# Performance work log

Measured on AMD Instinct MI355X. Metric: run time of the kernel, lower is better.

The kernel has to match this reference:

```python
import jax, jax.numpy as jnp
import numpy as np

H = 384  # LSTMCell features per layer
REVS = (True, False, True, False, True)  # reverse flags per layer (keep_order=True restores order)


def _lstm_layer(x, Wi, Wh, b, rev):
    # x: [B, T, D]; Wi: [D, 4H]; Wh: [H, 4H]; b: [4H]
    # flax nn.RNN(reverse=True, keep_order=True) == flip input, scan, flip output.
    if rev:
        x = x[:, ::-1]
    xT = jnp.swapaxes(x, 0, 1)            # [T, B, D]
    xproj = xT @ Wi + b                    # precompute input projection: [T, B, 4H]
    B = x.shape[0]
    c0 = jnp.zeros((B, H), x.dtype)
    h0 = jnp.zeros((B, H), x.dtype)

    def step(carry, xp):
        c, h = carry
        z = xp + h @ Wh                    # [B, 4H]
        i, f, g, o = jnp.split(z, 4, axis=-1)
        c = jax.nn.sigmoid(f) * c + jax.nn.sigmoid(i) * jnp.tanh(g)
        h = jax.nn.sigmoid(o) * jnp.tanh(c)
        return (c, h), h

    _, hs = jax.lax.scan(step, (c0, h0), xproj)  # hs: [T, B, H]
    out = jnp.swapaxes(hs, 0, 1)                 # [B, T, H]
    if rev:
        out = out[:, ::-1]
    return out


def setup_inputs() -> dict:
    key = jax.random.key(0)
    k_x, k_wi, k_wh = jax.random.split(key, 3)
    B, T, D = 64, 1024, 384
    x = jax.random.normal(k_x, (B, T, D), dtype=jnp.float32)
    # flax LSTMCell: input dense (no bias) + recurrent dense (with bias); bias init zeros.
    Wi = jax.random.normal(k_wi, (5, D, 4 * H), dtype=jnp.float32) * 0.05
    Wh = jax.random.normal(k_wh, (5, H, 4 * H), dtype=jnp.float32) * 0.05
    b = jnp.zeros((5, 4 * H), dtype=jnp.float32)
    return {"x": x, "Wi": Wi, "Wh": Wh, "b": b}


def reference(x, Wi, Wh, b):
    for l, rev in enumerate(REVS):
        x = _lstm_layer(x, Wi[l], Wh[l], b[l], rev)
    return x
```

## Files before the change

### kernel.cpp

```cpp
#include <hip/hip_runtime.h>
#include <cstdint>
#include <cstddef>


#define T_SEQ   1024
#define DD      384
#define HH      384
#define FH      1536
#define NBATCH  64
#define BG      8
#define CC      24
#define JHW     16
#define RTHREADS 512
#define SMEM_BYTES 129664

typedef unsigned long long u64;

__device__ __forceinline__ float sigmoidf_(float x) {
  return 1.0f / (1.0f + __expf(-x));
}
__device__ __forceinline__ float tanhf_(float x) {
  float ax = fabsf(x);
  float e  = __expf(-2.0f * ax);
  float r  = (1.0f - e) / (1.0f + e);
  return (x >= 0.0f) ? r : -r;
}

__global__ __launch_bounds__(256) void gemm_xproj(
    const float* __restrict__ xin, const float* __restrict__ Wi,
    const float* __restrict__ bias, float* __restrict__ xproj,
    int t0, int rev)
{
  __shared__ float As[8][132];
  __shared__ float Bs[8][132];

  const int tid = threadIdx.x;
  const int tx = tid & 15, ty = tid >> 4;
  const int m0 = blockIdx.y * 128;
  const int j0 = blockIdx.x * 128;

  const int r    = tid >> 1;
  const int part = tid & 1;
  const int m    = m0 + r;
  const int b    = m & 63;
  const int trel = m >> 6;
  const int t    = t0 + trel;
  const int tsrc = rev ? (T_SEQ - 1 - t) : t;
  const float* arow = xin + ((size_t)b * T_SEQ + tsrc) * DD + part * 4;

  const int kr = tid >> 5;
  const int jc = (tid & 31) << 2;
  const float* brow = Wi + (size_t)kr * FH + j0 + jc;

  float acc[8][8];
#pragma unroll
  for (int i = 0; i < 8; ++i)
#pragma unroll
    for (int j = 0; j < 8; ++j) acc[i][j] = 0.0f;

  for (int kt = 0; kt < 48; ++kt) {
    float4 av = *(const float4*)(arow + kt * 8);
    float4 bv = *(const float4*)(brow + (size_t)kt * 8 * FH);
    __syncthreads();
    As[part * 4 + 0][r] = av.x;
    As[part * 4 + 1][r] = av.y;
    As[part * 4 + 2][r] = av.z;
    As[part * 4 + 3][r] = av.w;
    *(float4*)&Bs[kr][jc] = bv;
    __syncthreads();
#pragma unroll
    for (int k = 0; k < 8; ++k) {
      float a[8], bb[8];
      *(float4*)&a[0]  = *(const float4*)&As[k][ty * 8];
      *(float4*)&a[4]  = *(const float4*)&As[k][ty * 8 + 4];
      *(float4*)&bb[0] = *(const float4*)&Bs[k][tx * 8];
      *(float4*)&bb[4] = *(const float4*)&Bs[k][tx * 8 + 4];
#pragma unroll
      for (int i = 0; i < 8; ++i)
#pragma unroll
        for (int j = 0; j < 8; ++j)
          acc[i][j] = fmaf(a[i], bb[j], acc[i][j]);
    }
  }

  float bvals[8];
#pragma unroll
  for (int j = 0; j < 8; ++j) bvals[j] = bias[j0 + tx * 8 + j];

#pragma unroll
  for (int i = 0; i < 8; ++i) {
    const int mm = m0 + ty * 8 + i;
    float* orow = xproj + (size_t)mm * FH + j0 + tx * 8;
    float4 o0, o1;
    o0.x = acc[i][0] + bvals[0]; o0.y = acc[i][1] + bvals[1];
    o0.z = acc[i][2] + bvals[2]; o0.w = acc[i][3] + bvals[3];
    o1.x = acc[i][4] + bvals[4]; o1.y = acc[i][5] + bvals[5];
    o1.z = acc[i][6] + bvals[6]; o1.w = acc[i][7] + bvals[7];
    *(float4*)(orow)     = o0;
    *(float4*)(orow + 4) = o1;
  }
}

__global__ __launch_bounds__(RTHREADS) void lstm_recur(
    const float* __restrict__ xp, const float* __restrict__ Wh,
    float* __restrict__ xout, u64* __restrict__ h_ex,
    float* __restrict__ c_state,
    int t0, int Tc, int rev, int layer)
{
  extern __shared__ char smem[];
  float (*WhL)[64]  = (float (*)[64])(smem);
  float (*hL)[388]  = (float (*)[388])(smem + 98304);
  float* zred       = (float*)(smem + 110720);
  float* cL         = (float*)(smem + 129152);

  const int wg   = blockIdx.x;
  const int bg   = wg / CC;
  const int cc   = wg % CC;
  const int tid  = threadIdx.x;
  const int wave = tid >> 6;
  const int lane = tid & 63;
  const unsigned base = (unsigned)(layer * 1025);

  for (int idx = tid; idx < 384 * 64; idx += RTHREADS) {
    int k = idx >> 6;
    int c = idx & 63;
    int col = ((c >> 4) * HH) + cc * JHW + (c & 15);
    WhL[k][c] = Wh[(size_t)k * FH + col];
  }

  const int rb    = tid >> 4;
  const int rjj   = tid & 15;
  const int bglob = bg * BG + rb;
  const int hb    = cc * JHW + rjj;

  if (tid < 128) {
    cL[tid] = (t0 == 0) ? 0.0f : c_state[(size_t)bglob * HH + hb];
    if (t0 == 0) {
      u64 pack = ((u64)base << 32);
      __hip_atomic_store(&h_ex[(size_t)(NBATCH * HH) + (size_t)bglob * HH + hb],
                         pack, __ATOMIC_RELAXED, __HIP_MEMORY_SCOPE_AGENT);
    }
  }
  __syncthreads();

  const int k0 = wave * 48;

  for (int tr = 0; tr < Tc; ++tr) {
    const int t = t0 + tr;

    float xpr0 = 0.f, xpr1 = 0.f, xpr2 = 0.f, xpr3 = 0.f;
    if (tid < 128) {
      const float* xr = xp + ((size_t)tr * NBATCH + bglob) * FH + cc * JHW + rjj;
      xpr0 = xr[0];
      xpr1 = xr[384];
      xpr2 = xr[768];
      xpr3 = xr[1152];
    }

    {
      const unsigned tagT = base + (unsigned)t;
      const u64* hsrc = h_ex + (size_t)((t + 1) & 1) * (NBATCH * HH)
                             + (size_t)bg * BG * HH;
      u64 v[6];
#pragma unroll
      for (int k = 0; k < 6; ++k)
        v[k] = __hip_atomic_load(&hsrc[tid + k * RTHREADS],
                                 __ATOMIC_RELAXED, __HIP_MEMORY_SCOPE_AGENT);
#pragma unroll
      for (int k = 0; k < 6; ++k) {
        while ((unsigned)(v[k] >> 32) != tagT) {
          v[k] = __hip_atomic_load(&hsrc[tid + k * RTHREADS],
                                   __ATOMIC_RELAXED, __HIP_MEMORY_SCOPE_AGENT);
        }
        const int e  = tid + k * RTHREADS;
        const int bb = e / HH;
        const int cl = e - bb * HH;
        hL[bb][cl] = __uint_as_float((unsigned)v[k]);
      }
    }
    __syncthreads();

    float acc[8] = {0, 0, 0, 0, 0, 0, 0, 0};
#pragma unroll 4
    for (int q = 0; q < 12; ++q) {
      const int k = k0 + q * 4;
      const float w0 = WhL[k][lane];
      const float w1 = WhL[k + 1][lane];
      const float w2 = WhL[k + 2][lane];
      const float w3 = WhL[k + 3][lane];
#pragma unroll
      for (int bb = 0; bb < 8; ++bb) {
        float4 h4 = *(const float4*)&hL[bb][k];
        acc[bb] = fmaf(w0, h4.x, acc[bb]);
        acc[bb] = fmaf(w1, h4.y, acc[bb]);
        acc[bb] = fmaf(w2, h4.z, acc[bb]);
        acc[bb] = fmaf(w3, h4.w, acc[bb]);
      }
    }
#pragma unroll
    for (int bb = 0; bb < 8; ++bb)
      zred[(bb * 64 + lane) * 9 + wave] = acc[bb];
    __syncthreads();

    if (tid < 128) {
      float zi = xpr0, zf = xpr1, zg = xpr2, zo = xpr3;
#pragma unroll
      for (int w = 0; w < 8; ++w) {
        zi += zred[(rb * 64 +  0 + rjj) * 9 + w];
        zf += zred[(rb * 64 + 16 + rjj) * 9 + w];
        zg += zred[(rb * 64 + 32 + rjj) * 9 + w];
        zo += zred[(rb * 64 + 48 + rjj) * 9 + w];
      }
      float c = cL[tid];
      c = sigmoidf_(zf) * c + sigmoidf_(zi) * tanhf_(zg);
      float h = sigmoidf_(zo) * tanhf_(c);
      cL[tid] = c;
      u64 pack = ((u64)(base + (unsigned)t + 1u) << 32)
               | (u64)__float_as_uint(h);
      __hip_atomic_store(&h_ex[(size_t)(t & 1) * (NBATCH * HH)
                               + (size_t)bglob * HH + hb],
                         pack, __ATOMIC_RELAXED, __HIP_MEMORY_SCOPE_AGENT);
      const int to = rev ? (T_SEQ - 1 - t) : t;
      xout[((size_t)bglob * T_SEQ + to) * HH + hb] = h;
    }
    __syncthreads();
  }

  if (tid < 128) {
    c_state[(size_t)bglob * HH + hb] = cL[tid];
  }
}

extern "C" void kernel_launch(void* const* d_in, const int* in_sizes, int n_in,
                              void* d_out, int out_size, void* d_ws, size_t ws_size,
                              hipStream_t stream) {
  (void)in_sizes; (void)n_in; (void)out_size;

  const float* x  = (const float*)d_in[0];
  const float* Wi = (const float*)d_in[1];
  const float* Wh = (const float*)d_in[2];
  const float* bs = (const float*)d_in[3];
  float* out = (float*)d_out;

  char*  ws      = (char*)d_ws;
  float* c_state = (float*)ws;
  u64*   h_ex    = (u64*)(ws + 98304);
  float* xproj   = (float*)(ws + 98304 + 393216);
  const size_t fixed = 98304 + 393216;

  int Tc = 1024;
  while (Tc > 8 && fixed + (size_t)Tc * NBATCH * FH * 4 > ws_size) Tc >>= 1;

  (void)hipFuncSetAttribute((const void*)lstm_recur,
                            hipFuncAttributeMaxDynamicSharedMemorySize,
                            SMEM_BYTES);

  const int revs[5] = {1, 0, 1, 0, 1};
  for (int l = 0; l < 5; ++l) {
    const float* xin = (l == 0) ? x : out;
    for (int t0 = 0; t0 < T_SEQ; t0 += Tc) {
      dim3 g(FH / 128, (unsigned)((Tc * NBATCH) / 128));
      gemm_xproj<<<g, 256, 0, stream>>>(xin, Wi + (size_t)l * DD * FH,
                                        bs + (size_t)l * FH, xproj, t0, revs[l]);
      lstm_recur<<<192, RTHREADS, SMEM_BYTES, stream>>>(
          xproj, Wh + (size_t)l * DD * FH, out, h_ex, c_state,
          t0, Tc, revs[l], l);
    }
  }
}
```

Before: 30.67 ms.

## Remap workgroups to XCDs, prefetch GEMM tiles, drop redundant recurrence barrier

```diff
diff --git a/kernel.cpp b/kernel.cpp
--- a/kernel.cpp
+++ b/kernel.cpp
@@ -36,8 +36,21 @@
 
   const int tid = threadIdx.x;
   const int tx = tid & 15, ty = tid >> 4;
-  const int m0 = blockIdx.y * 128;
-  const int j0 = blockIdx.x * 128;
+
+  const int nyb = gridDim.x / 12;
+  int bx, by;
+  if ((nyb & 7) == 0) {
+    const int xcd   = blockIdx.x & 7;
+    const int s     = blockIdx.x >> 3;
+    const int chunk = nyb >> 3;
+    by = xcd * chunk + s / 12;
+    bx = s % 12;
+  } else {
+    bx = blockIdx.x % 12;
+    by = blockIdx.x / 12;
+  }
+  const int m0 = by * 128;
+  const int j0 = bx * 128;
 
   const int r    = tid >> 1;
   const int part = tid & 1;
@@ -58,9 +71,10 @@
 #pragma unroll
     for (int j = 0; j < 8; ++j) acc[i][j] = 0.0f;
 
+  float4 av = *(const float4*)(arow);
+  float4 bv = *(const float4*)(brow);
+
   for (int kt = 0; kt < 48; ++kt) {
-    float4 av = *(const float4*)(arow + kt * 8);
-    float4 bv = *(const float4*)(brow + (size_t)kt * 8 * FH);
     __syncthreads();
     As[part * 4 + 0][r] = av.x;
     As[part * 4 + 1][r] = av.y;
@@ -68,6 +82,10 @@
     As[part * 4 + 3][r] = av.w;
     *(float4*)&Bs[kr][jc] = bv;
     __syncthreads();
+    if (kt < 47) {
+      av = *(const float4*)(arow + (kt + 1) * 8);
+      bv = *(const float4*)(brow + (size_t)(kt + 1) * 8 * FH);
+    }
 #pragma unroll
     for (int k = 0; k < 8; ++k) {
       float a[8], bb[8];
@@ -114,8 +132,8 @@
   float* cL         = (float*)(smem + 129152);
 
   const int wg   = blockIdx.x;
-  const int bg   = wg / CC;
-  const int cc   = wg % CC;
+  const int bg   = wg & 7;
+  const int cc   = wg >> 3;
   const int tid  = threadIdx.x;
   const int wave = tid >> 6;
   const int lane = tid & 63;
@@ -223,7 +241,6 @@
       const int to = rev ? (T_SEQ - 1 - t) : t;
       xout[((size_t)bglob * T_SEQ + to) * HH + hb] = h;
     }
-    __syncthreads();
   }
 
   if (tid < 128) {
@@ -259,9 +276,10 @@
   for (int l = 0; l < 5; ++l) {
     const float* xin = (l == 0) ? x : out;
     for (int t0 = 0; t0 < T_SEQ; t0 += Tc) {
-      dim3 g(FH / 128, (unsigned)((Tc * NBATCH) / 128));
-      gemm_xproj<<<g, 256, 0, stream>>>(xin, Wi + (size_t)l * DD * FH,
-                                        bs + (size_t)l * FH, xproj, t0, revs[l]);
+      const int nyb = (Tc * NBATCH) / 128;
+      gemm_xproj<<<dim3(nyb * 12), 256, 0, stream>>>(
+          xin, Wi + (size_t)l * DD * FH,
+          bs + (size_t)l * FH, xproj, t0, revs[l]);
       lstm_recur<<<192, RTHREADS, SMEM_BYTES, stream>>>(
           xproj, Wh + (size_t)l * DD * FH, out, h_ex, c_state,
           t0, Tc, revs[l], l);
```

Result: slower. 32.64 ms (+6.4%).
